# Kernel optimization log

Hardware: AMD Instinct MI355X
Metric: run time of the kernel (lower is better)

Reference implementation:

```python
import jax, jax.numpy as jnp
import numpy as np

B, L, H, D = 16, 2048, 768, 768
M, TPL = 8, 16  # labels per example, tokens per label


def setup_inputs() -> dict:
    key = jax.random.key(0)
    k1, k2, k3, k4 = jax.random.split(key, 4)
    hidden_states = jax.random.normal(k1, (B, L, H), dtype=jnp.float32)
    # first M*TPL tokens are label tokens with ids 1..M, rest are text tokens
    pos = jnp.arange(L)
    row = jnp.where(pos < M * TPL, pos // TPL + 1, 0).astype(jnp.int32)
    lmask = jnp.broadcast_to(row, (B, L))
    input_ids = jax.random.randint(k2, (B, L), 0, 30000, dtype=jnp.int32)
    attention_mask = jnp.ones((B, L), dtype=jnp.int32)
    Wt = jax.random.normal(k3, (H, D), dtype=jnp.float32) / np.sqrt(H)
    bt = jnp.zeros((D,), dtype=jnp.float32)
    Wl = jax.random.normal(k4, (H, D), dtype=jnp.float32) / np.sqrt(H)
    bl = jnp.zeros((D,), dtype=jnp.float32)
    attention_temperature = jnp.array(1.0, dtype=jnp.float32)
    logit_scale = jnp.array(2.0, dtype=jnp.float32)
    return dict(hidden_states=hidden_states, Wt=Wt, bt=bt, Wl=Wl, bl=bl,
                attention_temperature=attention_temperature, logit_scale=logit_scale,
                lmask=lmask, input_ids=input_ids, attention_mask=attention_mask,
                num_labels=M)


def reference(hidden_states, Wt, bt, Wl, bl, attention_temperature, logit_scale,
              lmask, input_ids, attention_mask, num_labels):
    # hidden_states: (B, L, H); lmask: (B, L) int label ids (>0 = label token)
    Bb, Ll, _ = hidden_states.shape
    Mm = num_labels  # static python int (== max label id)
    proj_text = hidden_states @ Wt + bt            # (B, L, D)  text_projector (dropout=eval identity)
    proj_label = hidden_states @ Wl + bl           # (B, L, D)  label_projector on all tokens
    label_tok = lmask > 0                          # (B, L)
    # segment-mean of projected label tokens per (batch, label_id) slot
    flat_idx = jnp.where(label_tok,
                         jnp.arange(Bb, dtype=lmask.dtype)[:, None] * Mm + (lmask - 1),
                         Bb * Mm).reshape(-1)
    masked = proj_label * label_tok[..., None].astype(proj_label.dtype)
    seg = jax.ops.segment_sum(masked.reshape(Bb * Ll, -1), flat_idx,
                              num_segments=Bb * Mm + 1)[: Bb * Mm]
    counts = jax.ops.segment_sum(label_tok.reshape(-1).astype(jnp.float32), flat_idx,
                                 num_segments=Bb * Mm + 1)[: Bb * Mm]
    aggregated_labels = seg / jnp.maximum(counts, 1.0)[:, None]   # (B*M, D)
    agg = aggregated_labels.reshape(Bb, Mm, -1)                   # (B, M, D)
    # attention-weighted text pooling per label over text tokens
    text_mask = (lmask == 0) & (attention_mask == 1)              # (B, L)
    temp = jnp.maximum(jnp.abs(attention_temperature), 0.1)
    scores = jnp.einsum('bmd,bld->bml', agg, proj_text) / temp
    scores = jnp.where(text_mask[:, None, :], scores, -jnp.inf)
    attn = jax.nn.softmax(scores, axis=-1)                        # (B, M, L)
    aggregated_text = jnp.einsum('bml,bld->bmd', attn, proj_text).reshape(Bb * Mm, -1)
    # cosine similarity head with learnable temperature exp(logit_scale)
    tn = aggregated_text / jnp.clip(jnp.linalg.norm(aggregated_text, axis=-1, keepdims=True), 1e-8)
    ln = aggregated_labels / jnp.clip(jnp.linalg.norm(aggregated_labels, axis=-1, keepdims=True), 1e-8)
    scale = jnp.exp(logit_scale)
    logits = jnp.sum(tn * ln, axis=-1, keepdims=True) * scale     # (B*M, 1)
    all_batch_ids = jnp.repeat(jnp.arange(Bb), Mm)
    all_label_ids = jnp.tile(jnp.arange(1, Mm + 1), Bb)
    return (logits, all_batch_ids, all_label_ids, aggregated_labels, scale, aggregated_text)
```

## Files before the change

### kernel.cpp

```cpp
#include <hip/hip_runtime.h>
#include <hip/hip_bf16.h>

typedef __attribute__((ext_vector_type(8))) short s16x8;
typedef __attribute__((ext_vector_type(4))) short s16x4;
typedef __attribute__((ext_vector_type(4))) float f32x4;

#define BB 16
#define LL 2048
#define HH 768
#define DD 768
#define MM 8
#define NCH 32

#define O_LOGITS 0
#define O_BID    128
#define O_LID    256
#define O_AGGL   384
#define O_SCALE  98688
#define O_AGGT   98689

#define WTT_OFF  0u
#define WLT_OFF  1179648u
#define WTB_OFF  2359296u
#define HBAR_OFF 3538944u
#define HST_OFF  4325376u
#define CVEC_OFF 4718592u
#define PML_OFF  4719104u
#define PO_OFF   4751872u
#define SK_OFF   17334784u

__device__ __forceinline__ short f2bf(float x) {
  union { float f; unsigned u; } v; v.f = x;
  unsigned r = v.u + 0x7FFFu + ((v.u >> 16) & 1u);
  return (short)(r >> 16);
}
__device__ __forceinline__ float bf2f(short x) {
  union { unsigned u; float f; } v; v.u = ((unsigned)(unsigned short)x) << 16;
  return v.f;
}

#define GLOAD_LDS16(gp, lp) __builtin_amdgcn_global_load_lds( \
    (const __attribute__((address_space(1))) unsigned int*)(gp), \
    (__attribute__((address_space(3))) unsigned int*)(lp), 16, 0, 0)

__global__ void k_prep(const float* __restrict__ Wt, const float* __restrict__ Wl,
                       short* __restrict__ Wtt, short* __restrict__ Wlt,
                       short* __restrict__ Wtb,
                       const float* __restrict__ hs, const int* __restrict__ lmask,
                       float* __restrict__ hbar) {
  __shared__ float tile[64][65];
  __shared__ int list[LL];
  __shared__ int nlist_s;
  int bx = blockIdx.x;
  int t = threadIdx.x;
  if (bx < 432) {
    int z = bx / 144, r = bx % 144;
    int kb = (r % 12) * 64, nb = (r / 12) * 64;
    int c = t & 63;
    int r0 = (t >> 6) * 16;
    if (z == 2) {
#pragma unroll
      for (int i = 0; i < 16; ++i) {
        int rr = kb + r0 + i;
        Wtb[(size_t)rr * DD + nb + c] = f2bf(Wt[(size_t)rr * DD + nb + c]);
      }
      return;
    }
    const float* src = z ? Wl : Wt;
    short* dst = z ? Wlt : Wtt;
#pragma unroll
    for (int i = 0; i < 16; ++i)
      tile[r0 + i][c] = src[(size_t)(kb + r0 + i) * DD + nb + c];
    __syncthreads();
#pragma unroll
    for (int i = 0; i < 16; ++i)
      dst[(size_t)(nb + r0 + i) * HH + kb + c] = f2bf(tile[c][r0 + i]);
    return;
  }
  int bh = bx - 432;
  int b = bh >> 3, m = bh & 7;
  int lane = t & 63, w = t >> 6;
  if (w == 0) {
    int base = 0;
    for (int win = 0; win < LL / 64; ++win) {
      int l = win * 64 + lane;
      bool match = (lmask[b * LL + l] == m + 1);
      unsigned long long mk = __ballot(match);
      if (match) {
        int pos = base + (int)__popcll(mk & ((1ull << lane) - 1ull));
        list[pos] = l;
      }
      base += (int)__popcll(mk);
    }
    if (lane == 0) nlist_s = base;
  }
  __syncthreads();
  int n = nlist_s;
  float inv = 1.0f / (float)(n > 1 ? n : 1);
  float a0 = 0.f, a1 = 0.f, a2 = 0.f;
  for (int i = 0; i < n; ++i) {
    const float* rr = hs + (size_t)(b * LL + list[i]) * HH;
    a0 += rr[t]; a1 += rr[t + 256]; a2 += rr[t + 512];
  }
  float* dst = hbar + (size_t)(b * MM + m) * HH;
  dst[t] = a0 * inv; dst[t + 256] = a1 * inv; dst[t + 512] = a2 * inv;
}

__global__ __launch_bounds__(256, 3)
void k_skgemm(const float* __restrict__ A, const short* __restrict__ Bt,
              float* __restrict__ part) {
  __shared__ short As[128][64];
  __shared__ short Bs[2][128][64];
  int t = threadIdx.x;
  int lane = t & 63, w = t >> 6;
  int wm = w >> 1, wn = w & 1;
  int n0 = blockIdx.x * 128;
  int kt0 = blockIdx.y * 3;

  f32x4 acc[4][4] = {};
  float4 areg[8];

  auto issueA = [&](int kt) {
    const float* Ag = A + (size_t)(kt0 + kt) * 64;
#pragma unroll
    for (int i = 0; i < 8; ++i) {
      int slot = i * 256 + t;
      int row = slot >> 4, c = slot & 15;
      areg[i] = *(const float4*)(Ag + (size_t)row * HH + c * 4);
    }
  };
  auto issueB = [&](int kt, int buf) {
    const short* Bg = Bt + (size_t)n0 * HH + (size_t)(kt0 + kt) * 64;
#pragma unroll
    for (int i = 0; i < 4; ++i) {
      int slot = i * 256 + w * 64 + lane;
      int row = slot >> 3, c = slot & 7;
      int cs = c ^ (row & 7);
      GLOAD_LDS16(Bg + (size_t)row * HH + cs * 8,
                  (char*)&Bs[0][0][0] + (size_t)buf * 16384 + (size_t)(i * 256 + w * 64) * 16);
    }
  };
  auto writeA = [&]() {
#pragma unroll
    for (int i = 0; i < 8; ++i) {
      int slot = i * 256 + t;
      int row = slot >> 4, c = slot & 15;
      unsigned d0, d1;
      asm("v_cvt_pk_bf16_f32 %0, %1, %2" : "=v"(d0) : "v"(areg[i].x), "v"(areg[i].y));
      asm("v_cvt_pk_bf16_f32 %0, %1, %2" : "=v"(d1) : "v"(areg[i].z), "v"(areg[i].w));
      int phys = (c >> 1) ^ (row & 7);
      uint2 val = {d0, d1};
      *(uint2*)((char*)&As[0][0] + (size_t)row * 128 + phys * 16 + (c & 1) * 8) = val;
    }
  };
  auto compute = [&](int buf) {
#pragma unroll
    for (int kk = 0; kk < 2; ++kk) {
      s16x8 a[4], bb[4];
#pragma unroll
      for (int i = 0; i < 4; ++i) {
        int row = wm * 64 + i * 16 + (lane & 15);
        int p = (kk * 4 + (lane >> 4)) ^ (row & 7);
        a[i] = *(const s16x8*)((const char*)&As[0][0] + (size_t)row * 128 + p * 16);
      }
#pragma unroll
      for (int i = 0; i < 4; ++i) {
        int row = wn * 64 + i * 16 + (lane & 15);
        int p = (kk * 4 + (lane >> 4)) ^ (row & 7);
        bb[i] = *(const s16x8*)((const char*)&Bs[0][0][0] + (size_t)buf * 16384 + (size_t)row * 128 + p * 16);
      }
#pragma unroll
      for (int mi = 0; mi < 4; ++mi)
#pragma unroll
        for (int ni = 0; ni < 4; ++ni)
          acc[mi][ni] = __builtin_amdgcn_mfma_f32_16x16x32_bf16(a[mi], bb[ni], acc[mi][ni], 0, 0, 0);
    }
  };

  issueA(0); issueB(0, 0);
  writeA();
  __syncthreads();
  for (int kt = 0; kt < 3; ++kt) {
    if (kt + 1 < 3) { issueA(kt + 1); issueB(kt + 1, (kt + 1) & 1); }
    compute(kt & 1);
    __syncthreads();
    if (kt + 1 < 3) {
      writeA();
      __syncthreads();
    }
  }

  float* po = part + (size_t)blockIdx.y * 128 * HH;
#pragma unroll
  for (int mi = 0; mi < 4; ++mi) {
    int row = wm * 64 + mi * 16 + ((lane >> 4) * 4);
#pragma unroll
    for (int ni = 0; ni < 4; ++ni) {
      int col = n0 + wn * 64 + ni * 16 + (lane & 15);
#pragma unroll
      for (int j = 0; j < 4; ++j)
        po[(size_t)(row + j) * HH + col] = acc[mi][ni][j];
    }
  }
}

__global__ void k_red_agg(const float* __restrict__ part, const float* __restrict__ bl,
                          const float* __restrict__ bt, float* __restrict__ out,
                          float* __restrict__ cvec) {
  int row = blockIdx.x;
  int t = threadIdx.x;
  int lane = t & 63, w = t >> 6;
  __shared__ float wred[4];
  float dotbt = 0.f;
#pragma unroll
  for (int cc = 0; cc < 3; ++cc) {
    int c = cc * 256 + t;
    float s = bl[c];
#pragma unroll
    for (int kc = 0; kc < 4; ++kc)
      s += part[((size_t)kc * 128 + row) * HH + c];
    out[O_AGGL + (size_t)row * DD + c] = s;
    dotbt += s * bt[c];
  }
  for (int sh = 32; sh; sh >>= 1) dotbt += __shfl_xor(dotbt, sh, 64);
  if (lane == 0) wred[w] = dotbt;
  __syncthreads();
  if (t == 0) cvec[row] = wred[0] + wred[1] + wred[2] + wred[3];
}

__global__ __launch_bounds__(512, 6)
void k_attnpool(const float* __restrict__ hs, const float* __restrict__ qhp,
                const float* __restrict__ cvec, const int* __restrict__ lmask,
                const int* __restrict__ amask, const float* __restrict__ temp_p,
                short* __restrict__ part_o, float* __restrict__ part_ml) {
  __shared__ short As[8][2][16][64];
  __shared__ short Bs[8][776];
  __shared__ float w_acc[4][64][4];
  __shared__ float w_lds[64][8];
  int chunk = blockIdx.x;
  int b = blockIdx.y;
  int t = threadIdx.x;
  int lane = t & 63, w = t >> 6;
  int wq = w & 3, kw = w >> 2;

  for (int c = t; c < HH; c += 512) {
#pragma unroll
    for (int r = 0; r < 8; ++r) {
      size_t o = (size_t)(b * MM + r) * HH + c;
      float s = qhp[o] + qhp[(size_t)128 * HH + o] + qhp[(size_t)256 * HH + o] + qhp[(size_t)384 * HH + o];
      Bs[r][c] = f2bf(s);
    }
  }

  const float* Hg = hs + (size_t)(b * LL + chunk * 64) * HH;
  const float* Wrow = Hg + (size_t)(wq * 16) * HH;
  int kbase = kw * 384;
  bool brow_ok = (lane & 15) < MM;
  float4 areg[2][4];

  auto issueA = [&](int set, int kt) {
#pragma unroll
    for (int i = 0; i < 4; ++i) {
      int slot = i * 64 + lane;
      int row = slot >> 4, c = slot & 15;
      if (set == 0)
        areg[0][i] = *(const float4*)(Wrow + (size_t)row * HH + kbase + kt * 64 + c * 4);
      else
        areg[1][i] = *(const float4*)(Wrow + (size_t)row * HH + kbase + kt * 64 + c * 4);
    }
  };
  auto writeA = [&](int set, int buf) {
#pragma unroll
    for (int i = 0; i < 4; ++i) {
      int slot = i * 64 + lane;
      int row = slot >> 4, c = slot & 15;
      float4 v = set == 0 ? areg[0][i] : areg[1][i];
      unsigned d0, d1;
      asm("v_cvt_pk_bf16_f32 %0, %1, %2" : "=v"(d0) : "v"(v.x), "v"(v.y));
      asm("v_cvt_pk_bf16_f32 %0, %1, %2" : "=v"(d1) : "v"(v.z), "v"(v.w));
      int phys = (c >> 1) ^ (row & 7);
      uint2 val = {d0, d1};
      *(uint2*)((char*)&As[w][buf][0][0] + (size_t)row * 128 + phys * 16 + (c & 1) * 8) = val;
    }
  };

  f32x4 acc = {};
  issueA(0, 0); issueA(1, 1);
  writeA(0, 0);
  __syncthreads();
#pragma unroll
  for (int kt = 0; kt < 6; ++kt) {
    int buf = kt & 1;
#pragma unroll
    for (int kk = 0; kk < 2; ++kk) {
      int r = lane & 15;
      int p = (kk * 4 + (lane >> 4)) ^ (r & 7);
      s16x8 a = *(const s16x8*)((const char*)&As[w][buf][0][0] + (size_t)r * 128 + p * 16);
      s16x8 braw = *(const s16x8*)&Bs[r & 7][kbase + kt * 64 + kk * 32 + (lane >> 4) * 8];
      s16x8 bfr = brow_ok ? braw : (s16x8){0, 0, 0, 0, 0, 0, 0, 0};
      acc = __builtin_amdgcn_mfma_f32_16x16x32_bf16(a, bfr, acc, 0, 0, 0);
    }
    if (kt + 1 < 6) writeA((kt + 1) & 1, (kt + 1) & 1);
    if (kt + 2 < 6) issueA(kt & 1, kt + 2);
  }

  if (kw == 1) {
    w_acc[wq][lane][0] = acc[0]; w_acc[wq][lane][1] = acc[1];
    w_acc[wq][lane][2] = acc[2]; w_acc[wq][lane][3] = acc[3];
  }
  __syncthreads();
  if (kw == 0) {
    acc[0] += w_acc[wq][lane][0]; acc[1] += w_acc[wq][lane][1];
    acc[2] += w_acc[wq][lane][2]; acc[3] += w_acc[wq][lane][3];
  }

  float inv_temp = 1.0f / fmaxf(fabsf(temp_p[0]), 0.1f);
  int m = lane & 15;
  int tok0 = wq * 16 + (lane >> 4) * 4;
  if (kw == 0 && m < MM) {
    float cv = cvec[b * MM + m];
    int4 lm = *(const int4*)&lmask[b * LL + chunk * 64 + tok0];
    int4 am = *(const int4*)&amask[b * LL + chunk * 64 + tok0];
    w_lds[tok0 + 0][m] = (lm.x == 0 && am.x == 1) ? (acc[0] + cv) * inv_temp : -1e30f;
    w_lds[tok0 + 1][m] = (lm.y == 0 && am.y == 1) ? (acc[1] + cv) * inv_temp : -1e30f;
    w_lds[tok0 + 2][m] = (lm.z == 0 && am.z == 1) ? (acc[2] + cv) * inv_temp : -1e30f;
    w_lds[tok0 + 3][m] = (lm.w == 0 && am.w == 1) ? (acc[3] + cv) * inv_temp : -1e30f;
  }
  __syncthreads();

  {
    float v = w_lds[lane][w];
    float mx = v;
    for (int s = 32; s; s >>= 1) mx = fmaxf(mx, __shfl_xor(mx, s, 64));
    float e = __expf(v - mx);
    float l = e;
    for (int s = 32; s; s >>= 1) l += __shfl_xor(l, s, 64);
    w_lds[lane][w] = e;
    if (lane == 0) {
      float* pml = part_ml + ((size_t)(chunk * BB + b) * MM + w) * 2;
      pml[0] = mx; pml[1] = l;
    }
  }
  __syncthreads();

  if (t < 384) {
    int h0 = t * 2;
    float2 o[8] = {};
    const float* hp = Hg + h0;
#pragma unroll 4
    for (int tok = 0; tok < 64; ++tok) {
      float2 hv = *(const float2*)(hp + (size_t)tok * HH);
      float4 w0 = *(const float4*)&w_lds[tok][0];
      float4 w1 = *(const float4*)&w_lds[tok][4];
      o[0].x += w0.x * hv.x; o[0].y += w0.x * hv.y;
      o[1].x += w0.y * hv.x; o[1].y += w0.y * hv.y;
      o[2].x += w0.z * hv.x; o[2].y += w0.z * hv.y;
      o[3].x += w0.w * hv.x; o[3].y += w0.w * hv.y;
      o[4].x += w1.x * hv.x; o[4].y += w1.x * hv.y;
      o[5].x += w1.y * hv.x; o[5].y += w1.y * hv.y;
      o[6].x += w1.z * hv.x; o[6].y += w1.z * hv.y;
      o[7].x += w1.w * hv.x; o[7].y += w1.w * hv.y;
    }
    short* po = part_o + (size_t)(chunk * BB + b) * MM * HH + h0;
#pragma unroll
    for (int mm = 0; mm < 8; ++mm) {
      short2 pv = {f2bf(o[mm].x), f2bf(o[mm].y)};
      *(short2*)(po + (size_t)mm * HH) = pv;
    }
  }
}

__global__ void k_finish(const short* __restrict__ part_o, const float* __restrict__ part_ml,
                         float* __restrict__ hst) {
  int row = blockIdx.x;
  int b = row >> 3, m = row & 7;
  int t = threadIdx.x;
  float mg = -1e30f;
#pragma unroll
  for (int lc = 0; lc < NCH; ++lc)
    mg = fmaxf(mg, part_ml[((size_t)(lc * BB + b) * MM + m) * 2]);
  float L = 0.f;
  f32x4 acc = {};
  int h0 = t * 4;
#pragma unroll 4
  for (int lc = 0; lc < NCH; ++lc) {
    const float* pml = part_ml + ((size_t)(lc * BB + b) * MM + m) * 2;
    float f = __expf(pml[0] - mg);
    L += pml[1] * f;
    s16x4 v = *(const s16x4*)(part_o + ((size_t)(lc * BB + b) * MM + m) * HH + h0);
    acc[0] += bf2f(v[0]) * f; acc[1] += bf2f(v[1]) * f;
    acc[2] += bf2f(v[2]) * f; acc[3] += bf2f(v[3]) * f;
  }
  float inv = 1.0f / L;
  f32x4 r = {acc[0] * inv, acc[1] * inv, acc[2] * inv, acc[3] * inv};
  *(f32x4*)(hst + (size_t)row * HH + h0) = r;
}

__global__ void k_head(const float* __restrict__ part, const float* __restrict__ bt,
                       const float* __restrict__ lscale_p, float* __restrict__ out) {
  int row = blockIdx.x;
  int lane = threadIdx.x;
  const float* al = out + O_AGGL + (size_t)row * DD;
  float dot = 0.f, nt = 0.f, nl = 0.f;
  for (int i = lane; i < DD; i += 64) {
    float a = bt[i];
#pragma unroll
    for (int kc = 0; kc < 4; ++kc)
      a += part[((size_t)kc * 128 + row) * HH + i];
    out[O_AGGT + (size_t)row * DD + i] = a;
    float c = al[i];
    dot += a * c; nt += a * a; nl += c * c;
  }
  for (int s = 32; s; s >>= 1) {
    dot += __shfl_xor(dot, s, 64);
    nt  += __shfl_xor(nt, s, 64);
    nl  += __shfl_xor(nl, s, 64);
  }
  if (lane == 0) {
    float scale = expf(lscale_p[0]);
    float denom = fmaxf(sqrtf(nt), 1e-8f) * fmaxf(sqrtf(nl), 1e-8f);
    out[O_LOGITS + row] = dot / denom * scale;
    out[O_BID + row] = (float)(row >> 3);
    out[O_LID + row] = (float)((row & 7) + 1);
    if (row == 0) out[O_SCALE] = scale;
  }
}

extern "C" void kernel_launch(void* const* d_in, const int* in_sizes, int n_in,
                              void* d_out, int out_size, void* d_ws, size_t ws_size,
                              hipStream_t stream) {
  const float* hs    = (const float*)d_in[0];
  const float* Wt    = (const float*)d_in[1];
  const float* bt    = (const float*)d_in[2];
  const float* Wl    = (const float*)d_in[3];
  const float* bl    = (const float*)d_in[4];
  const float* atemp = (const float*)d_in[5];
  const float* lsc   = (const float*)d_in[6];
  const int*   lmask = (const int*)d_in[7];
  const int*   amask = (const int*)d_in[9];
  float* out = (float*)d_out;
  char* ws = (char*)d_ws;
  short* Wtt  = (short*)(ws + WTT_OFF);
  short* Wlt  = (short*)(ws + WLT_OFF);
  short* Wtb  = (short*)(ws + WTB_OFF);
  float* hbar = (float*)(ws + HBAR_OFF);
  float* hst  = (float*)(ws + HST_OFF);
  float* cvec = (float*)(ws + CVEC_OFF);
  float* pml  = (float*)(ws + PML_OFF);
  short* po   = (short*)(ws + PO_OFF);
  float* skp  = (float*)(ws + SK_OFF);

  k_prep<<<560, 256, 0, stream>>>(Wt, Wl, Wtt, Wlt, Wtb, hs, lmask, hbar);
  k_skgemm<<<dim3(6, 4), 256, 0, stream>>>(hbar, Wlt, skp);
  k_red_agg<<<128, 256, 0, stream>>>(skp, bl, bt, out, cvec);
  k_skgemm<<<dim3(6, 4), 256, 0, stream>>>(out + O_AGGL, Wtb, skp);
  k_attnpool<<<dim3(NCH, 16), 512, 0, stream>>>(hs, skp, cvec, lmask, amask, atemp, po, pml);
  k_finish<<<128, 192, 0, stream>>>(po, pml, hst);
  k_skgemm<<<dim3(6, 4), 256, 0, stream>>>(hst, Wtt, skp);
  k_head<<<128, 64, 0, stream>>>(skp, bt, lsc, out);
}
```

Measured before the change: 83.49 us.

## Stage hidden chunk once in LDS as bf16 and reuse for pooling pass

The attention-pool kernel now loads its whole token chunk of hidden states into shared memory as bf16 once, and uses that copy both for the score MFMA and for the weighted pooling pass. Previously the chunk was streamed through per-wave double buffers and then re-read from global memory in fp32 for pooling. The chunk shrinks from 64 to 32 tokens, which doubles the grid to 64 chunks, and the K split widens to four ways with a three-way LDS reduction. The cost is more LDS per block, lower occupancy (launch bounds drop from 6 to 4), more partial outputs for the finish kernel to merge, and pooling on bf16-rounded activations, which loses precision.

```diff
diff --git a/kernel.cpp b/kernel.cpp
--- a/kernel.cpp
+++ b/kernel.cpp
@@ -10,7 +10,8 @@
 #define HH 768
 #define DD 768
 #define MM 8
-#define NCH 32
+#define TOKS 32
+#define NCH 64
 
 #define O_LOGITS 0
 #define O_BID    128
@@ -26,8 +27,8 @@
 #define HST_OFF  4325376u
 #define CVEC_OFF 4718592u
 #define PML_OFF  4719104u
-#define PO_OFF   4751872u
-#define SK_OFF   17334784u
+#define PO_OFF   4784640u
+#define SK_OFF   17367552u
 
 __device__ __forceinline__ short f2bf(float x) {
   union { float f; unsigned u; } v; v.f = x;
@@ -228,20 +229,20 @@
   if (t == 0) cvec[row] = wred[0] + wred[1] + wred[2] + wred[3];
 }
 
-__global__ __launch_bounds__(512, 6)
+__global__ __launch_bounds__(512, 4)
 void k_attnpool(const float* __restrict__ hs, const float* __restrict__ qhp,
                 const float* __restrict__ cvec, const int* __restrict__ lmask,
                 const int* __restrict__ amask, const float* __restrict__ temp_p,
                 short* __restrict__ part_o, float* __restrict__ part_ml) {
-  __shared__ short As[8][2][16][64];
+  __shared__ short Hs[TOKS][768];
   __shared__ short Bs[8][776];
-  __shared__ float w_acc[4][64][4];
-  __shared__ float w_lds[64][8];
+  __shared__ float w_acc[2][3][64][4];
+  __shared__ float w_lds[TOKS][8];
   int chunk = blockIdx.x;
   int b = blockIdx.y;
   int t = threadIdx.x;
   int lane = t & 63, w = t >> 6;
-  int wq = w & 3, kw = w >> 2;
+  int tq = w & 1, kq = w >> 1;
 
   for (int c = t; c < HH; c += 512) {
 #pragma unroll
@@ -252,75 +253,62 @@
     }
   }
 
-  const float* Hg = hs + (size_t)(b * LL + chunk * 64) * HH;
-  const float* Wrow = Hg + (size_t)(wq * 16) * HH;
-  int kbase = kw * 384;
+  const float* Hg = hs + (size_t)(b * LL + chunk * TOKS) * HH;
+#pragma unroll
+  for (int i = 0; i < 6; ++i) {
+    int slot = i * 512 + t;
+    int row = slot / 96, c = slot % 96;
+    const float* src = Hg + (size_t)row * HH + c * 8;
+    float4 x0 = *(const float4*)src;
+    float4 x1 = *(const float4*)(src + 4);
+    unsigned d0, d1, d2, d3;
+    asm("v_cvt_pk_bf16_f32 %0, %1, %2" : "=v"(d0) : "v"(x0.x), "v"(x0.y));
+    asm("v_cvt_pk_bf16_f32 %0, %1, %2" : "=v"(d1) : "v"(x0.z), "v"(x0.w));
+    asm("v_cvt_pk_bf16_f32 %0, %1, %2" : "=v"(d2) : "v"(x1.x), "v"(x1.y));
+    asm("v_cvt_pk_bf16_f32 %0, %1, %2" : "=v"(d3) : "v"(x1.z), "v"(x1.w));
+    int phys = c ^ (row & 7);
+    uint4 val = {d0, d1, d2, d3};
+    *(uint4*)((char*)&Hs[0][0] + (size_t)row * 1536 + phys * 16) = val;
+  }
+  __syncthreads();
+
   bool brow_ok = (lane & 15) < MM;
-  float4 areg[2][4];
-
-  auto issueA = [&](int set, int kt) {
-#pragma unroll
-    for (int i = 0; i < 4; ++i) {
-      int slot = i * 64 + lane;
-      int row = slot >> 4, c = slot & 15;
-      if (set == 0)
-        areg[0][i] = *(const float4*)(Wrow + (size_t)row * HH + kbase + kt * 64 + c * 4);
-      else
-        areg[1][i] = *(const float4*)(Wrow + (size_t)row * HH + kbase + kt * 64 + c * 4);
-    }
-  };
-  auto writeA = [&](int set, int buf) {
-#pragma unroll
-    for (int i = 0; i < 4; ++i) {
-      int slot = i * 64 + lane;
-      int row = slot >> 4, c = slot & 15;
-      float4 v = set == 0 ? areg[0][i] : areg[1][i];
-      unsigned d0, d1;
-      asm("v_cvt_pk_bf16_f32 %0, %1, %2" : "=v"(d0) : "v"(v.x), "v"(v.y));
-      asm("v_cvt_pk_bf16_f32 %0, %1, %2" : "=v"(d1) : "v"(v.z), "v"(v.w));
-      int phys = (c >> 1) ^ (row & 7);
-      uint2 val = {d0, d1};
-      *(uint2*)((char*)&As[w][buf][0][0] + (size_t)row * 128 + phys * 16 + (c & 1) * 8) = val;
-    }
-  };
-
+  int arow = tq * 16 + (lane & 15);
   f32x4 acc = {};
-  issueA(0, 0); issueA(1, 1);
-  writeA(0, 0);
-  __syncthreads();
-#pragma unroll
-  for (int kt = 0; kt < 6; ++kt) {
-    int buf = kt & 1;
+#pragma unroll
+  for (int kt = 0; kt < 3; ++kt) {
 #pragma unroll
     for (int kk = 0; kk < 2; ++kk) {
-      int r = lane & 15;
-      int p = (kk * 4 + (lane >> 4)) ^ (r & 7);
-      s16x8 a = *(const s16x8*)((const char*)&As[w][buf][0][0] + (size_t)r * 128 + p * 16);
-      s16x8 braw = *(const s16x8*)&Bs[r & 7][kbase + kt * 64 + kk * 32 + (lane >> 4) * 8];
+      int c = kq * 24 + kt * 8 + kk * 4 + (lane >> 4);
+      int phys = c ^ (arow & 7);
+      s16x8 a = *(const s16x8*)((const char*)&Hs[0][0] + (size_t)arow * 1536 + phys * 16);
+      int koff = kq * 192 + kt * 64 + kk * 32 + (lane >> 4) * 8;
+      s16x8 braw = *(const s16x8*)&Bs[(lane & 15) & 7][koff];
       s16x8 bfr = brow_ok ? braw : (s16x8){0, 0, 0, 0, 0, 0, 0, 0};
       acc = __builtin_amdgcn_mfma_f32_16x16x32_bf16(a, bfr, acc, 0, 0, 0);
     }
-    if (kt + 1 < 6) writeA((kt + 1) & 1, (kt + 1) & 1);
-    if (kt + 2 < 6) issueA(kt & 1, kt + 2);
-  }
-
-  if (kw == 1) {
-    w_acc[wq][lane][0] = acc[0]; w_acc[wq][lane][1] = acc[1];
-    w_acc[wq][lane][2] = acc[2]; w_acc[wq][lane][3] = acc[3];
-  }
-  __syncthreads();
-  if (kw == 0) {
-    acc[0] += w_acc[wq][lane][0]; acc[1] += w_acc[wq][lane][1];
-    acc[2] += w_acc[wq][lane][2]; acc[3] += w_acc[wq][lane][3];
+  }
+
+  if (kq > 0) {
+    w_acc[tq][kq - 1][lane][0] = acc[0]; w_acc[tq][kq - 1][lane][1] = acc[1];
+    w_acc[tq][kq - 1][lane][2] = acc[2]; w_acc[tq][kq - 1][lane][3] = acc[3];
+  }
+  __syncthreads();
+  if (kq == 0) {
+#pragma unroll
+    for (int q = 0; q < 3; ++q) {
+      acc[0] += w_acc[tq][q][lane][0]; acc[1] += w_acc[tq][q][lane][1];
+      acc[2] += w_acc[tq][q][lane][2]; acc[3] += w_acc[tq][q][lane][3];
+    }
   }
 
   float inv_temp = 1.0f / fmaxf(fabsf(temp_p[0]), 0.1f);
   int m = lane & 15;
-  int tok0 = wq * 16 + (lane >> 4) * 4;
-  if (kw == 0 && m < MM) {
+  int tok0 = tq * 16 + (lane >> 4) * 4;
+  if (kq == 0 && m < MM) {
     float cv = cvec[b * MM + m];
-    int4 lm = *(const int4*)&lmask[b * LL + chunk * 64 + tok0];
-    int4 am = *(const int4*)&amask[b * LL + chunk * 64 + tok0];
+    int4 lm = *(const int4*)&lmask[b * LL + chunk * TOKS + tok0];
+    int4 am = *(const int4*)&amask[b * LL + chunk * TOKS + tok0];
     w_lds[tok0 + 0][m] = (lm.x == 0 && am.x == 1) ? (acc[0] + cv) * inv_temp : -1e30f;
     w_lds[tok0 + 1][m] = (lm.y == 0 && am.y == 1) ? (acc[1] + cv) * inv_temp : -1e30f;
     w_lds[tok0 + 2][m] = (lm.z == 0 && am.z == 1) ? (acc[2] + cv) * inv_temp : -1e30f;
@@ -329,13 +317,13 @@
   __syncthreads();
 
   {
-    float v = w_lds[lane][w];
+    float v = (lane < TOKS) ? w_lds[lane][w] : -1e30f;
     float mx = v;
     for (int s = 32; s; s >>= 1) mx = fmaxf(mx, __shfl_xor(mx, s, 64));
-    float e = __expf(v - mx);
+    float e = (lane < TOKS) ? __expf(v - mx) : 0.f;
     float l = e;
     for (int s = 32; s; s >>= 1) l += __shfl_xor(l, s, 64);
-    w_lds[lane][w] = e;
+    if (lane < TOKS) w_lds[lane][w] = e;
     if (lane == 0) {
       float* pml = part_ml + ((size_t)(chunk * BB + b) * MM + w) * 2;
       pml[0] = mx; pml[1] = l;
@@ -344,23 +332,27 @@
   __syncthreads();
 
   if (t < 384) {
-    int h0 = t * 2;
+    int cch = t >> 2;
+    int within = ((t * 2) & 7) * 2;
     float2 o[8] = {};
-    const float* hp = Hg + h0;
 #pragma unroll 4
-    for (int tok = 0; tok < 64; ++tok) {
-      float2 hv = *(const float2*)(hp + (size_t)tok * HH);
+    for (int tok = 0; tok < TOKS; ++tok) {
+      int phys = cch ^ (tok & 7);
+      unsigned pv = *(const unsigned*)((const char*)&Hs[0][0] + (size_t)tok * 1536 + phys * 16 + within);
+      float hx = bf2f((short)(pv & 0xffff));
+      float hy = bf2f((short)(pv >> 16));
       float4 w0 = *(const float4*)&w_lds[tok][0];
       float4 w1 = *(const float4*)&w_lds[tok][4];
-      o[0].x += w0.x * hv.x; o[0].y += w0.x * hv.y;
-      o[1].x += w0.y * hv.x; o[1].y += w0.y * hv.y;
-      o[2].x += w0.z * hv.x; o[2].y += w0.z * hv.y;
-      o[3].x += w0.w * hv.x; o[3].y += w0.w * hv.y;
-      o[4].x += w1.x * hv.x; o[4].y += w1.x * hv.y;
-      o[5].x += w1.y * hv.x; o[5].y += w1.y * hv.y;
-      o[6].x += w1.z * hv.x; o[6].y += w1.z * hv.y;
-      o[7].x += w1.w * hv.x; o[7].y += w1.w * hv.y;
-    }
+      o[0].x += w0.x * hx; o[0].y += w0.x * hy;
+      o[1].x += w0.y * hx; o[1].y += w0.y * hy;
+      o[2].x += w0.z * hx; o[2].y += w0.z * hy;
+      o[3].x += w0.w * hx; o[3].y += w0.w * hy;
+      o[4].x += w1.x * hx; o[4].y += w1.x * hy;
+      o[5].x += w1.y * hx; o[5].y += w1.y * hy;
+      o[6].x += w1.z * hx; o[6].y += w1.z * hy;
+      o[7].x += w1.w * hx; o[7].y += w1.w * hy;
+    }
+    int h0 = t * 2;
     short* po = part_o + (size_t)(chunk * BB + b) * MM * HH + h0;
 #pragma unroll
     for (int mm = 0; mm < 8; ++mm) {
```

After: 83.44 us. About the same (-0.1%).
